# Kernel optimization log

Measured on AMD Instinct MI355X. Metric: run time of the kernel, lower is better.

The kernel has to match this reference:

```python
import jax, jax.numpy as jnp
import numpy as np

T, WAY, SHOT, QUERY, C = 4, 16, 8, 256, 256

def setup_inputs() -> dict:
    key = jax.random.key(0)
    k1, k2, k3 = jax.random.split(key, 3)
    query_feat = jax.random.normal(k1, (T, WAY * QUERY, C), dtype=jnp.float32)
    support_feat = jax.random.normal(k2, (T, WAY * SHOT, C), dtype=jnp.float32)
    support_target = jax.random.randint(k3, (T, WAY * SHOT), 0, WAY, dtype=jnp.int64)
    return {
        "query_feat": query_feat,
        "support_feat": support_feat,
        "support_target": support_target,
        "way_num": WAY,
        "shot_num": SHOT,
        "query_num": QUERY,
    }

def reference(query_feat, support_feat, support_target, way_num, shot_num, query_num):
    t, wq, c = query_feat.shape
    # prototype = mean over shots: (t, way, shot, c) -> (t, way, c)
    proto_feat = jnp.mean(
        support_feat.reshape(t, way_num, shot_num, c), axis=2
    )
    q = query_feat.reshape(t, way_num * query_num, c)
    # negative squared euclidean distance: (t, wq, way)
    diff = q[:, :, None, :] - proto_feat[:, None, :, :]  # (t, wq, way, c)
    return -jnp.sum(diff * diff, axis=3)
```

## Files before the change

### kernel.cpp

```cpp
#include <hip/hip_runtime.h>


constexpr int T_    = 4;
constexpr int WAY   = 16;
constexpr int SHOT  = 8;
constexpr int C     = 256;
constexpr int WQ    = 4096;
constexpr int C4    = C / 4;
constexpr int PITCH = 260;

__global__ __launch_bounds__(256) void proto_kernel(
    const float* __restrict__ support,
    float* __restrict__ proto)
{
    const int t       = blockIdx.x >> 2;
    const int quarter = blockIdx.x & 3;
    const int idx     = quarter * 256 + threadIdx.x;
    const int w  = idx >> 6;
    const int c4 = idx & 63;

    const float4* row = (const float4*)(support + (size_t)t * (WAY * SHOT * C))
                        + (w * SHOT) * C4 + c4;
    float4 s = make_float4(0.f, 0.f, 0.f, 0.f);
    #pragma unroll
    for (int sh = 0; sh < SHOT; ++sh) {
        float4 v = row[sh * C4];
        s.x += v.x; s.y += v.y; s.z += v.z; s.w += v.w;
    }
    s.x *= 0.125f; s.y *= 0.125f; s.z *= 0.125f; s.w *= 0.125f;

    float4* dst = (float4*)(proto + (size_t)t * (WAY * C));
    dst[w * C4 + c4] = s;
}

__global__ __launch_bounds__(128) void dist_kernel(
    const float* __restrict__ query,
    const float* __restrict__ proto,
    float* __restrict__ out)
{
    __shared__ float ps[WAY * PITCH];
    __shared__ float qs[32  * PITCH];

    const int tid = threadIdx.x;
    const int t   = blockIdx.x >> 7;
    const int qb  = (blockIdx.x & 127) * 32;

    {
        const float4* src = (const float4*)(proto + (size_t)t * (WAY * C));
        #pragma unroll
        for (int i = 0; i < 8; ++i) {
            int idx = tid + i * 128;
            int w = idx >> 6, c4 = idx & 63;
            float4 v = src[idx];
            *(float4*)&ps[w * PITCH + c4 * 4] = v;
        }
    }
    {
        const float4* src = (const float4*)(query + ((size_t)t * WQ + qb) * C);
        #pragma unroll
        for (int i = 0; i < 16; ++i) {
            int idx = tid + i * 128;
            int q = idx >> 6, c4 = idx & 63;
            float4 v = src[idx];
            *(float4*)&qs[q * PITCH + c4 * 4] = v;
        }
    }
    __syncthreads();

    const int ql = tid >> 3;
    const int wg = (tid & 7) * 2;

    const float* q0 = &qs[(2 * ql + 0) * PITCH];
    const float* q1 = &qs[(2 * ql + 1) * PITCH];
    const float* p0 = &ps[(wg + 0) * PITCH];
    const float* p1 = &ps[(wg + 1) * PITCH];

    float a00 = 0.f, a01 = 0.f, a10 = 0.f, a11 = 0.f;
    #pragma unroll 8
    for (int c = 0; c < C; c += 4) {
        float4 qa = *(const float4*)(q0 + c);
        float4 qv = *(const float4*)(q1 + c);
        float4 pa = *(const float4*)(p0 + c);
        float4 pb = *(const float4*)(p1 + c);

        float d;
        d = qa.x - pa.x; a00 += d * d;
        d = qa.y - pa.y; a00 += d * d;
        d = qa.z - pa.z; a00 += d * d;
        d = qa.w - pa.w; a00 += d * d;

        d = qa.x - pb.x; a01 += d * d;
        d = qa.y - pb.y; a01 += d * d;
        d = qa.z - pb.z; a01 += d * d;
        d = qa.w - pb.w; a01 += d * d;

        d = qv.x - pa.x; a10 += d * d;
        d = qv.y - pa.y; a10 += d * d;
        d = qv.z - pa.z; a10 += d * d;
        d = qv.w - pa.w; a10 += d * d;

        d = qv.x - pb.x; a11 += d * d;
        d = qv.y - pb.y; a11 += d * d;
        d = qv.z - pb.z; a11 += d * d;
        d = qv.w - pb.w; a11 += d * d;
    }

    float* ob = out + (((size_t)t * WQ + qb + 2 * ql) * WAY + wg);
    *(float2*)ob         = make_float2(-a00, -a01);
    *(float2*)(ob + WAY) = make_float2(-a10, -a11);
}

extern "C" void kernel_launch(void* const* d_in, const int* in_sizes, int n_in,
                              void* d_out, int out_size, void* d_ws, size_t ws_size,
                              hipStream_t stream) {
    const float* query   = (const float*)d_in[0];
    const float* support = (const float*)d_in[1];
    float* out   = (float*)d_out;
    float* proto = (float*)d_ws;

    proto_kernel<<<dim3(T_ * 4), 256, 0, stream>>>(support, proto);
    dist_kernel <<<dim3(T_ * 128), 128, 0, stream>>>(query, proto, out);
}
```

Measured before the change: 79.04 us.

## Load tiles via global_load_lds and widen per-thread tile to 2x4

Staging of query and prototype tiles into shared memory now uses direct global-to-LDS loads (global_load_lds, 16 bytes per lane), so data no longer passes through registers. The distance block shrinks to 64 threads, and each thread computes 2 queries by 4 prototypes, which raises register reuse of LDS reads and allows float4 output stores. The risk is that one wave per block with large LDS use leaves little parallelism to hide latency. The 16-byte global_load_lds variant also needs hardware support, and LDS placement of the padded rows depends on the builtin's addressing semantics.

```diff
diff --git a/kernel.cpp b/kernel.cpp
--- a/kernel.cpp
+++ b/kernel.cpp
@@ -8,6 +8,12 @@
 constexpr int WQ    = 4096;
 constexpr int C4    = C / 4;
 constexpr int PITCH = 260;
+
+__device__ __forceinline__ void g2lds16(const float4* g, float* lds) {
+    __builtin_amdgcn_global_load_lds(
+        (const __attribute__((address_space(1))) void*)g,
+        (__attribute__((address_space(3))) void*)lds, 16, 0, 0);
+}
 
 __global__ __launch_bounds__(256) void proto_kernel(
     const float* __restrict__ support,
@@ -29,11 +35,10 @@
     }
     s.x *= 0.125f; s.y *= 0.125f; s.z *= 0.125f; s.w *= 0.125f;
 
-    float4* dst = (float4*)(proto + (size_t)t * (WAY * C));
-    dst[w * C4 + c4] = s;
+    ((float4*)(proto + (size_t)t * (WAY * C)))[idx] = s;
 }
 
-__global__ __launch_bounds__(128) void dist_kernel(
+__global__ __launch_bounds__(64) void dist_kernel(
     const float* __restrict__ query,
     const float* __restrict__ proto,
     float* __restrict__ out)
@@ -45,69 +50,52 @@
     const int t   = blockIdx.x >> 7;
     const int qb  = (blockIdx.x & 127) * 32;
 
-    {
-        const float4* src = (const float4*)(proto + (size_t)t * (WAY * C));
-        #pragma unroll
-        for (int i = 0; i < 8; ++i) {
-            int idx = tid + i * 128;
-            int w = idx >> 6, c4 = idx & 63;
-            float4 v = src[idx];
-            *(float4*)&ps[w * PITCH + c4 * 4] = v;
-        }
-    }
-    {
-        const float4* src = (const float4*)(query + ((size_t)t * WQ + qb) * C);
-        #pragma unroll
-        for (int i = 0; i < 16; ++i) {
-            int idx = tid + i * 128;
-            int q = idx >> 6, c4 = idx & 63;
-            float4 v = src[idx];
-            *(float4*)&qs[q * PITCH + c4 * 4] = v;
-        }
-    }
+    const float4* psrc = (const float4*)(proto + (size_t)t * (WAY * C));
+    const float4* qsrc = (const float4*)(query + ((size_t)t * WQ + qb) * C);
+    #pragma unroll
+    for (int i = 0; i < WAY; ++i)
+        g2lds16(psrc + i * C4 + tid, &ps[i * PITCH]);
+    #pragma unroll
+    for (int i = 0; i < 32; ++i)
+        g2lds16(qsrc + i * C4 + tid, &qs[i * PITCH]);
     __syncthreads();
 
-    const int ql = tid >> 3;
-    const int wg = (tid & 7) * 2;
+    const int qp = tid >> 2;
+    const int wg = (tid & 3) * 4;
 
-    const float* q0 = &qs[(2 * ql + 0) * PITCH];
-    const float* q1 = &qs[(2 * ql + 1) * PITCH];
+    const float* q0 = &qs[qp * PITCH];
+    const float* q1 = &qs[(qp + 16) * PITCH];
     const float* p0 = &ps[(wg + 0) * PITCH];
     const float* p1 = &ps[(wg + 1) * PITCH];
+    const float* p2 = &ps[(wg + 2) * PITCH];
+    const float* p3 = &ps[(wg + 3) * PITCH];
 
-    float a00 = 0.f, a01 = 0.f, a10 = 0.f, a11 = 0.f;
+    float a0[4] = {0.f, 0.f, 0.f, 0.f};
+    float a1[4] = {0.f, 0.f, 0.f, 0.f};
+
     #pragma unroll 8
     for (int c = 0; c < C; c += 4) {
         float4 qa = *(const float4*)(q0 + c);
         float4 qv = *(const float4*)(q1 + c);
-        float4 pa = *(const float4*)(p0 + c);
-        float4 pb = *(const float4*)(p1 + c);
-
-        float d;
-        d = qa.x - pa.x; a00 += d * d;
-        d = qa.y - pa.y; a00 += d * d;
-        d = qa.z - pa.z; a00 += d * d;
-        d = qa.w - pa.w; a00 += d * d;
-
-        d = qa.x - pb.x; a01 += d * d;
-        d = qa.y - pb.y; a01 += d * d;
-        d = qa.z - pb.z; a01 += d * d;
-        d = qa.w - pb.w; a01 += d * d;
-
-        d = qv.x - pa.x; a10 += d * d;
-        d = qv.y - pa.y; a10 += d * d;
-        d = qv.z - pa.z; a10 += d * d;
-        d = qv.w - pa.w; a10 += d * d;
-
-        d = qv.x - pb.x; a11 += d * d;
-        d = qv.y - pb.y; a11 += d * d;
-        d = qv.z - pb.z; a11 += d * d;
-        d = qv.w - pb.w; a11 += d * d;
+        const float* pw[4] = {p0 + c, p1 + c, p2 + c, p3 + c};
+        #pragma unroll
+        for (int j = 0; j < 4; ++j) {
+            float4 pv = *(const float4*)pw[j];
+            float d;
+            d = qa.x - pv.x; a0[j] += d * d;
+            d = qa.y - pv.y; a0[j] += d * d;
+            d = qa.z - pv.z; a0[j] += d * d;
+            d = qa.w - pv.w; a0[j] += d * d;
+            d = qv.x - pv.x; a1[j] += d * d;
+            d = qv.y - pv.y; a1[j] += d * d;
+            d = qv.z - pv.z; a1[j] += d * d;
+            d = qv.w - pv.w; a1[j] += d * d;
+        }
     }
 
-    float* ob = out + (((size_t)t * WQ + qb + 2 * ql) * WAY + wg);
-    *(float2*)ob         = make_float2(-a00, -a01);
-    *(float2*)(ob + WAY) = make_float2(-a10, -a11);
+    float* ob = out + (((size_t)t * WQ + qb + qp) * WAY + wg);
+    *(float4*)ob              = make_float4(-a0[0], -a0[1], -a0[2], -a0[3]);
+    *(float4*)(ob + 16 * WAY) = make_float4(-a1[0], -a1[1], -a1[2], -a1[3]);
 }
 
 extern "C" void kernel_launch(void* const* d_in, const int* in_sizes, int n_in,
@@ -119,5 +107,5 @@
     float* proto = (float*)d_ws;
 
     proto_kernel<<<dim3(T_ * 4), 256, 0, stream>>>(support, proto);
-    dist_kernel <<<dim3(T_ * 128), 128, 0, stream>>>(query, proto, out);
+    dist_kernel <<<dim3(T_ * 128), 64, 0, stream>>>(query, proto, out);
 }
```

Result: slower. 81.99 us (+3.7%).
